# Kernel tuning notes

Measured on AMD Instinct MI355X. Metric: run time of the kernel, lower is better.

Reference implementation:

```python
import jax, jax.numpy as jnp
import numpy as np
from jax import lax

TAU = 0.1
TAU_BASE = 0.1
DIR_W = 1.0
N_LEVELS = 3  # labels has N_LEVELS hierarchy cols + 1 direction col
B, D = 4096, 1024


def setup_inputs() -> dict:
    key = jax.random.key(0)
    k1, k2 = jax.random.split(key)
    embeddings = jax.random.normal(k1, (B, D), dtype=jnp.float32)
    labels = jax.random.randint(k2, (B, N_LEVELS + 1), 0, 8, dtype=jnp.int64)
    return {"embeddings": embeddings, "labels": labels}


def _hier_loss(embeddings, labels):
    # F.normalize(dim=1) with eps=1e-12
    norm = jnp.linalg.norm(embeddings, axis=1, keepdims=True)
    z = embeddings / jnp.maximum(norm, 1e-12)
    hier = labels[:, :-1]          # [B, n_levels]
    dirs = labels[:, -1]           # [B]
    n_levels = hier.shape[1]
    b = z.shape[0]
    eye = jnp.eye(b, dtype=bool)

    sim = (z @ z.T) / TAU                                   # [B, B]
    sim = sim - lax.stop_gradient(jnp.max(sim, axis=1, keepdims=True))
    diff_dir = (dirs[:, None] != dirs[None, :])
    sim = sim - DIR_W * diff_dir.astype(sim.dtype)
    sim = jnp.where(eye, -jnp.inf, sim)
    tiny = jnp.finfo(sim.dtype).tiny
    log_prob = sim - jnp.log(jnp.maximum(jnp.exp(sim).sum(axis=1, keepdims=True), tiny))

    same_dir = ~diff_dir
    total = jnp.zeros((), dtype=sim.dtype)
    max_lower = jnp.full((), -jnp.inf, dtype=sim.dtype)
    seen = jnp.zeros((), dtype=jnp.int32)

    for lvl in range(1, n_levels + 1):  # small fixed loop over hierarchy levels
        same_up_to = jnp.all(hier[:, None, :lvl] == hier[None, :, :lvl], axis=2)  # [B, B]
        pos_mask = same_up_to & same_dir & ~eye
        pos_counts = pos_mask.sum(axis=1)                   # [B] int
        valid = pos_counts > 0
        num_valid = valid.sum()
        any_valid = num_valid > 0

        masked_logp = jnp.where(pos_mask, log_prob, 0.0)
        per_row = masked_logp.sum(axis=1) / jnp.maximum(pos_counts, 1).astype(sim.dtype)
        mean_logp_pos = jnp.sum(jnp.where(valid, per_row, 0.0)) / jnp.maximum(num_valid, 1).astype(sim.dtype)
        raw_loss = -(TAU / TAU_BASE) * mean_logp_pos

        # hmce: running max over levels (max_lower is detached)
        level_loss = jnp.maximum(max_lower, raw_loss)
        max_lower = jnp.where(any_valid,
                              lax.stop_gradient(jnp.maximum(max_lower, level_loss)),
                              max_lower)
        penalty = 2.0 ** (1.0 / lvl)  # h_penalty(1/lvl)
        total = total + jnp.where(any_valid, level_loss * penalty, 0.0)
        seen = seen + any_valid.astype(jnp.int32)

    return total / jnp.maximum(seen, 1).astype(total.dtype)


def reference(embeddings, labels):
    return _hier_loss(embeddings, labels)
```

## Files before the change

### kernel.cpp

```cpp
#include <hip/hip_runtime.h>
#include <hip/hip_bf16.h>
#include <stdint.h>

#define NB 4096
#define ND 1024

typedef __attribute__((ext_vector_type(4))) float f32x4;
typedef __attribute__((ext_vector_type(2))) long i64x2;

__global__ __launch_bounds__(256) void prep_kernel(
    const float* __restrict__ emb, const int* __restrict__ labels,
    unsigned char* __restrict__ zq, int* __restrict__ keys)
{
    const int wid = threadIdx.x >> 6, lane = threadIdx.x & 63;
    const int row = blockIdx.x * 4 + wid;
    const float4* src = (const float4*)(emb + (size_t)row * ND) + lane * 4;
    float4 v[4];
    float ss = 0.0f;
    #pragma unroll
    for (int j = 0; j < 4; ++j) {
        v[j] = src[j];
        ss += v[j].x * v[j].x + v[j].y * v[j].y + v[j].z * v[j].z + v[j].w * v[j].w;
    }
    #pragma unroll
    for (int o = 1; o < 64; o <<= 1) ss += __shfl_xor(ss, o);
    const float inv = 1.0f / fmaxf(sqrtf(ss), 1e-12f);

    int p0 = 0, p1 = 0, p2 = 0, p3 = 0;
    p0 = __builtin_amdgcn_cvt_pk_fp8_f32(v[0].x * inv, v[0].y * inv, p0, false);
    p0 = __builtin_amdgcn_cvt_pk_fp8_f32(v[0].z * inv, v[0].w * inv, p0, true);
    p1 = __builtin_amdgcn_cvt_pk_fp8_f32(v[1].x * inv, v[1].y * inv, p1, false);
    p1 = __builtin_amdgcn_cvt_pk_fp8_f32(v[1].z * inv, v[1].w * inv, p1, true);
    p2 = __builtin_amdgcn_cvt_pk_fp8_f32(v[2].x * inv, v[2].y * inv, p2, false);
    p2 = __builtin_amdgcn_cvt_pk_fp8_f32(v[2].z * inv, v[2].w * inv, p2, true);
    p3 = __builtin_amdgcn_cvt_pk_fp8_f32(v[3].x * inv, v[3].y * inv, p3, false);
    p3 = __builtin_amdgcn_cvt_pk_fp8_f32(v[3].z * inv, v[3].w * inv, p3, true);

    const int sf  = (row >> 4) * 16 + (lane >> 2);
    const int sel = (lane >> 1) & 1;
    const int c0  = (lane & 1) * 2;
    const int L0  = (row & 15) + 16 * c0;
    unsigned char* d = zq + (size_t)sf * 1024;
    int2 w01; w01.x = p0; w01.y = p1;
    int2 w23; w23.x = p2; w23.y = p3;
    *(int2*)(d + L0 * 16 + sel * 8)        = w01;
    *(int2*)(d + (L0 + 16) * 16 + sel * 8) = w23;

    if (lane == 0) {
        const int* lr = labels + row * 4;
        keys[row] = ((lr[3] & 7) << 24) | ((lr[0] & 7) << 16) |
                    ((lr[1] & 7) << 8)  |  (lr[2] & 7);
    }
}

__global__ __launch_bounds__(64, 4) void simtile_kernel(
    const unsigned char* __restrict__ zq, const int* __restrict__ keys,
    float* __restrict__ partials)
{
    const int b = blockIdx.x;
    const int p = (b & 7) * 260 + (b >> 3);
    int r = (int)((sqrtf(8.0f * p + 1.0f) - 1.0f) * 0.5f);
    while ((r + 1) * (r + 2) / 2 <= p) ++r;
    while (r * (r + 1) / 2 > p) --r;
    const int bi = p - r * (r + 1) / 2;
    const int bj = r;
    const int I0 = bi * 64, J0 = bj * 64;
    const bool offdiag = (bi != bj);
    const bool diag = !offdiag;

    const int lane = threadIdx.x;
    const int llo = lane & 15, lhi = lane >> 4;

    __shared__ int keyI[64];
    __shared__ int keyJ[64];
    keyI[lane] = keys[I0 + lane];
    keyJ[lane] = keys[J0 + lane];
    __syncthreads();

    const unsigned char* aF = zq + (size_t)(bi * 4) * 16384 + lane * 16;
    const unsigned char* bF = zq + (size_t)(bj * 4) * 16384 + lane * 16;

    f32x4 acc[4][4];
    #pragma unroll
    for (int m = 0; m < 4; ++m)
        #pragma unroll
        for (int n = 0; n < 4; ++n)
            acc[m][n] = (f32x4){0.f, 0.f, 0.f, 0.f};

    #pragma unroll 1
    for (int t = 0; t < 16; ++t) {
        i64x2 a[4], bb[4];
        #pragma unroll
        for (int m = 0; m < 4; ++m)
            a[m] = *(const i64x2*)(aF + (size_t)m * 16384 + (size_t)t * 1024);
        #pragma unroll
        for (int n = 0; n < 4; ++n)
            bb[n] = *(const i64x2*)(bF + (size_t)n * 16384 + (size_t)t * 1024);
        #pragma unroll
        for (int m = 0; m < 4; ++m)
            #pragma unroll
            for (int n = 0; n < 4; ++n) {
                acc[m][n] = __builtin_amdgcn_mfma_f32_16x16x32_fp8_fp8(
                    a[m][0], bb[n][0], acc[m][n], 0, 0, 0);
                acc[m][n] = __builtin_amdgcn_mfma_f32_16x16x32_fp8_fp8(
                    a[m][1], bb[n][1], acc[m][n], 0, 0, 0);
            }
    }

    int kJ[4], tcol[4];
    #pragma unroll
    for (int n = 0; n < 4; ++n) {
        tcol[n] = n * 16 + llo;
        kJ[n] = keyJ[tcol[n]];
    }

    float stB[4][4];
    #pragma unroll
    for (int n = 0; n < 4; ++n)
        #pragma unroll
        for (int s = 0; s < 4; ++s) stB[n][s] = 0.0f;

    #pragma unroll
    for (int m = 0; m < 4; ++m) {
        float stA[4][4];
        #pragma unroll
        for (int rr = 0; rr < 4; ++rr)
            #pragma unroll
            for (int s = 0; s < 4; ++s) stA[rr][s] = 0.0f;

        int kI[4], trow[4];
        #pragma unroll
        for (int rr = 0; rr < 4; ++rr) {
            trow[rr] = m * 16 + lhi * 4 + rr;
            kI[rr] = keyI[trow[rr]];
        }
        #pragma unroll
        for (int n = 0; n < 4; ++n) {
            #pragma unroll
            for (int rr = 0; rr < 4; ++rr) {
                const float v = acc[m][n][rr] * 10.0f;
                const int x = kI[rr] ^ kJ[n];
                const float pen = (x & 0xFF000000) ? 1.0f : 0.0f;
                const float g = __expf(v - 10.0f - pen);
                if (!(diag && trow[rr] == tcol[n])) {
                    stA[rr][0] += g;           stB[n][0] += g;
                    if ((x & 0xFFFF0000) == 0) { stA[rr][1] += v; stB[n][1] += v; }
                    if ((x & 0xFFFFFF00) == 0) { stA[rr][2] += v; stB[n][2] += v; }
                    if (x == 0)                { stA[rr][3] += v; stB[n][3] += v; }
                }
            }
        }
        #pragma unroll
        for (int rr = 0; rr < 4; ++rr)
            #pragma unroll
            for (int s = 0; s < 4; ++s) {
                float vv = stA[rr][s];
                vv += __shfl_xor(vv, 1);
                vv += __shfl_xor(vv, 2);
                vv += __shfl_xor(vv, 4);
                vv += __shfl_xor(vv, 8);
                stA[rr][s] = vv;
            }
        if (llo == 0) {
            #pragma unroll
            for (int rr = 0; rr < 4; ++rr) {
                float4 o; o.x = stA[rr][0]; o.y = stA[rr][1]; o.z = stA[rr][2]; o.w = stA[rr][3];
                *(float4*)(partials + ((size_t)bj * NB + I0 + trow[rr]) * 4) = o;
            }
        }
    }
    #pragma unroll
    for (int n = 0; n < 4; ++n)
        #pragma unroll
        for (int s = 0; s < 4; ++s) {
            float vv = stB[n][s];
            vv += __shfl_xor(vv, 16);
            vv += __shfl_xor(vv, 32);
            stB[n][s] = vv;
        }
    if (lhi == 0 && offdiag) {
        #pragma unroll
        for (int n = 0; n < 4; ++n) {
            float4 o; o.x = stB[n][0]; o.y = stB[n][1]; o.z = stB[n][2]; o.w = stB[n][3];
            *(float4*)(partials + ((size_t)bi * NB + J0 + tcol[n]) * 4) = o;
        }
    }
}

__global__ __launch_bounds__(256) void rowreduce_kernel(
    const float* __restrict__ partials, const int* __restrict__ keys,
    float* __restrict__ blocksums)
{
    const int tid = threadIdx.x;
    const int row = blockIdx.x * 256 + tid;
    const int lane = tid & 63, wid = tid >> 6;

    __shared__ int h3[4096];
    __shared__ int h2[512];
    __shared__ int h1[64];

    for (int i = tid; i < 4096; i += 256) h3[i] = 0;
    __syncthreads();
    for (int i = tid; i < 4096; i += 256) {
        const int k = keys[i];
        const int i3 = (((((k >> 24) & 7) * 8 + ((k >> 16) & 7)) * 8 + ((k >> 8) & 7)) * 8) + (k & 7);
        atomicAdd(&h3[i3], 1);
    }
    __syncthreads();
    for (int i = tid; i < 512; i += 256) {
        int s = 0;
        #pragma unroll
        for (int j = 0; j < 8; ++j) s += h3[i * 8 + j];
        h2[i] = s;
    }
    __syncthreads();
    if (tid < 64) {
        int s = 0;
        #pragma unroll
        for (int j = 0; j < 8; ++j) s += h2[tid * 8 + j];
        h1[tid] = s;
    }
    __syncthreads();

    float G = 0.f, T1 = 0.f, T2 = 0.f, T3 = 0.f;
    for (int ct = 0; ct < 64; ++ct) {
        const float4 u = *(const float4*)(partials + ((size_t)ct * NB + row) * 4);
        G += u.x; T1 += u.y; T2 += u.z; T3 += u.w;
    }
    const float lg = logf(fmaxf(G, 1e-30f)) + 10.0f;

    const int key = keys[row];
    const int i1 = ((key >> 24) & 7) * 8 + ((key >> 16) & 7);
    const int i2 = i1 * 8 + ((key >> 8) & 7);
    const int i3 = i2 * 8 + (key & 7);
    const int C[3] = {h1[i1] - 1, h2[i2] - 1, h3[i3] - 1};
    const float T[3] = {T1, T2, T3};

    float vals[6];
    #pragma unroll
    for (int l = 0; l < 3; ++l) {
        const bool valid = C[l] > 0;
        const float pr = T[l] / fmaxf((float)C[l], 1.0f) - lg;
        vals[2 * l]     = valid ? pr : 0.0f;
        vals[2 * l + 1] = valid ? 1.0f : 0.0f;
    }

    __shared__ float red[4][6];
    #pragma unroll
    for (int s = 0; s < 6; ++s) {
        float v = vals[s];
        #pragma unroll
        for (int o = 32; o > 0; o >>= 1) v += __shfl_xor(v, o);
        vals[s] = v;
    }
    if (lane == 0)
        #pragma unroll
        for (int s = 0; s < 6; ++s) red[wid][s] = vals[s];
    __syncthreads();
    if (tid == 0) {
        #pragma unroll
        for (int s = 0; s < 6; ++s)
            blocksums[blockIdx.x * 8 + s] = red[0][s] + red[1][s] + red[2][s] + red[3][s];
    }
}

__global__ void final_kernel(const float* __restrict__ blocksums, float* __restrict__ out)
{
    if (threadIdx.x != 0) return;
    float sums[6] = {0, 0, 0, 0, 0, 0};
    for (int b = 0; b < 16; ++b)
        for (int s = 0; s < 6; ++s) sums[s] += blocksums[b * 8 + s];

    const float pen[3] = {2.0f, 1.41421356237309515f, 1.25992104989487319f};
    float total = 0.0f, max_lower = -INFINITY;
    int seen = 0;
    for (int l = 0; l < 3; ++l) {
        const float nv   = sums[2 * l + 1];
        const bool  any  = nv > 0.0f;
        const float mean = sums[2 * l] / fmaxf(nv, 1.0f);
        const float raw  = -mean;
        const float lvl  = fmaxf(max_lower, raw);
        if (any) {
            total += lvl * pen[l];
            max_lower = fmaxf(max_lower, lvl);
            seen++;
        }
    }
    out[0] = total / (float)(seen > 0 ? seen : 1);
}

extern "C" void kernel_launch(void* const* d_in, const int* in_sizes, int n_in,
                              void* d_out, int out_size, void* d_ws, size_t ws_size,
                              hipStream_t stream)
{
    const float* emb    = (const float*)d_in[0];
    const int*   labels = (const int*)d_in[1];
    float*       out    = (float*)d_out;
    char*        ws     = (char*)d_ws;

    unsigned char* zq    = (unsigned char*)(ws);
    int*   keys     = (int*)(ws + 4194304);
    float* partials = (float*)(ws + 4210688);
    float* bsums    = (float*)(ws + 8404992);

    prep_kernel<<<NB / 4, 256, 0, stream>>>(emb, labels, zq, keys);
    simtile_kernel<<<2080, 64, 0, stream>>>(zq, keys, partials);
    rowreduce_kernel<<<NB / 256, 256, 0, stream>>>(partials, keys, bsums);
    final_kernel<<<1, 64, 0, stream>>>(bsums, out);
}
```

Measured before the change: 55.50 us.

## Use 128x128 tiles with four waves sharing double-buffered LDS fp8 panels

The similarity kernel moves from 64x64 tiles handled by one wave to 128x128 tiles handled by four waves. Each wave stages part of the A/B fp8 panels through double-buffered shared memory, so operands are shared across waves instead of each wave reading them from global memory. Per-row partial statistics are combined in shared memory before being written out, which halves the partials buffer and the row-reduce loop. The cost is fewer blocks (528), barrier overhead on every k-step, and more diagonal-tile waste.

Measured after the change: 51.41 us. 7.4% less time.

```diff
diff --git a/kernel.cpp b/kernel.cpp
--- a/kernel.cpp
+++ b/kernel.cpp
@@ -53,32 +53,54 @@
     }
 }
 
-__global__ __launch_bounds__(64, 4) void simtile_kernel(
+__global__ __launch_bounds__(256, 2) void simtile_kernel(
     const unsigned char* __restrict__ zq, const int* __restrict__ keys,
     float* __restrict__ partials)
 {
     const int b = blockIdx.x;
-    const int p = (b & 7) * 260 + (b >> 3);
+    const int p = (b & 7) * 66 + (b >> 3);
     int r = (int)((sqrtf(8.0f * p + 1.0f) - 1.0f) * 0.5f);
     while ((r + 1) * (r + 2) / 2 <= p) ++r;
     while (r * (r + 1) / 2 > p) --r;
     const int bi = p - r * (r + 1) / 2;
     const int bj = r;
-    const int I0 = bi * 64, J0 = bj * 64;
+    const int I0 = bi * 128, J0 = bj * 128;
     const bool offdiag = (bi != bj);
     const bool diag = !offdiag;
 
-    const int lane = threadIdx.x;
+    const int tid = threadIdx.x;
+    const int lane = tid & 63, w = tid >> 6;
     const int llo = lane & 15, lhi = lane >> 4;
-
-    __shared__ int keyI[64];
-    __shared__ int keyJ[64];
-    keyI[lane] = keys[I0 + lane];
-    keyJ[lane] = keys[J0 + lane];
-    __syncthreads();
-
-    const unsigned char* aF = zq + (size_t)(bi * 4) * 16384 + lane * 16;
-    const unsigned char* bF = zq + (size_t)(bj * 4) * 16384 + lane * 16;
+    const int wm = w >> 1, wn = w & 1;
+
+    __shared__ __align__(16) unsigned char sfb[2][16][1024];
+    __shared__ float epiA[2][128][4];
+    __shared__ float epiB[2][128][4];
+    __shared__ int keyI[128];
+    __shared__ int keyJ[128];
+
+    if (tid < 128) {
+        keyI[tid] = keys[I0 + tid];
+        keyJ[tid] = keys[J0 + tid];
+    }
+
+    const unsigned char* gpanel = (w < 2)
+        ? (zq + (size_t)(bi * 8 + w * 4) * 16384 + lane * 16)
+        : (zq + (size_t)(bj * 8 + (w - 2) * 4) * 16384 + lane * 16);
+
+    i64x2 stg[4];
+    #define GLOADU(T)                                                              \
+        do {                                                                       \
+            _Pragma("unroll")                                                      \
+            for (int q = 0; q < 4; ++q)                                            \
+                stg[q] = *(const i64x2*)(gpanel + (size_t)q * 16384 + (T) * 1024); \
+        } while (0)
+    #define DSWRITE(B)                                                             \
+        do {                                                                       \
+            _Pragma("unroll")                                                      \
+            for (int q = 0; q < 4; ++q)                                            \
+                *(i64x2*)(&sfb[B][w * 4 + q][lane * 16]) = stg[q];                 \
+        } while (0)
 
     f32x4 acc[4][4];
     #pragma unroll
@@ -87,15 +109,21 @@
         for (int n = 0; n < 4; ++n)
             acc[m][n] = (f32x4){0.f, 0.f, 0.f, 0.f};
 
+    GLOADU(0);
+    DSWRITE(0);
+    __syncthreads();
+
     #pragma unroll 1
     for (int t = 0; t < 16; ++t) {
+        const int buf = t & 1;
         i64x2 a[4], bb[4];
         #pragma unroll
         for (int m = 0; m < 4; ++m)
-            a[m] = *(const i64x2*)(aF + (size_t)m * 16384 + (size_t)t * 1024);
+            a[m] = *(const i64x2*)(&sfb[buf][wm * 4 + m][lane * 16]);
         #pragma unroll
         for (int n = 0; n < 4; ++n)
-            bb[n] = *(const i64x2*)(bF + (size_t)n * 16384 + (size_t)t * 1024);
+            bb[n] = *(const i64x2*)(&sfb[buf][8 + wn * 4 + n][lane * 16]);
+        if (t < 15) GLOADU(t + 1);
         #pragma unroll
         for (int m = 0; m < 4; ++m)
             #pragma unroll
@@ -105,12 +133,16 @@
                 acc[m][n] = __builtin_amdgcn_mfma_f32_16x16x32_fp8_fp8(
                     a[m][1], bb[n][1], acc[m][n], 0, 0, 0);
             }
-    }
+        if (t < 15) DSWRITE(buf ^ 1);
+        __syncthreads();
+    }
+    #undef GLOADU
+    #undef DSWRITE
 
     int kJ[4], tcol[4];
     #pragma unroll
     for (int n = 0; n < 4; ++n) {
-        tcol[n] = n * 16 + llo;
+        tcol[n] = wn * 64 + n * 16 + llo;
         kJ[n] = keyJ[tcol[n]];
     }
 
@@ -131,7 +163,7 @@
         int kI[4], trow[4];
         #pragma unroll
         for (int rr = 0; rr < 4; ++rr) {
-            trow[rr] = m * 16 + lhi * 4 + rr;
+            trow[rr] = wm * 64 + m * 16 + lhi * 4 + rr;
             kI[rr] = keyI[trow[rr]];
         }
         #pragma unroll
@@ -165,7 +197,7 @@
             #pragma unroll
             for (int rr = 0; rr < 4; ++rr) {
                 float4 o; o.x = stA[rr][0]; o.y = stA[rr][1]; o.z = stA[rr][2]; o.w = stA[rr][3];
-                *(float4*)(partials + ((size_t)bj * NB + I0 + trow[rr]) * 4) = o;
+                *(float4*)&epiA[wn][trow[rr]][0] = o;
             }
         }
     }
@@ -178,11 +210,25 @@
             vv += __shfl_xor(vv, 32);
             stB[n][s] = vv;
         }
-    if (lhi == 0 && offdiag) {
+    if (lhi == 0) {
         #pragma unroll
         for (int n = 0; n < 4; ++n) {
             float4 o; o.x = stB[n][0]; o.y = stB[n][1]; o.z = stB[n][2]; o.w = stB[n][3];
-            *(float4*)(partials + ((size_t)bi * NB + J0 + tcol[n]) * 4) = o;
+            *(float4*)&epiB[wm][tcol[n]][0] = o;
+        }
+    }
+    __syncthreads();
+
+    if (tid < 128) {
+        const float4 a0 = *(const float4*)&epiA[0][tid][0];
+        const float4 a1 = *(const float4*)&epiA[1][tid][0];
+        float4 o; o.x = a0.x + a1.x; o.y = a0.y + a1.y; o.z = a0.z + a1.z; o.w = a0.w + a1.w;
+        *(float4*)(partials + ((size_t)bj * NB + I0 + tid) * 4) = o;
+        if (offdiag) {
+            const float4 b0 = *(const float4*)&epiB[0][tid][0];
+            const float4 b1 = *(const float4*)&epiB[1][tid][0];
+            float4 q; q.x = b0.x + b1.x; q.y = b0.y + b1.y; q.z = b0.z + b1.z; q.w = b0.w + b1.w;
+            *(float4*)(partials + ((size_t)bi * NB + J0 + tid) * 4) = q;
         }
     }
 }
@@ -223,7 +269,7 @@
     __syncthreads();
 
     float G = 0.f, T1 = 0.f, T2 = 0.f, T3 = 0.f;
-    for (int ct = 0; ct < 64; ++ct) {
+    for (int ct = 0; ct < 32; ++ct) {
         const float4 u = *(const float4*)(partials + ((size_t)ct * NB + row) * 4);
         G += u.x; T1 += u.y; T2 += u.z; T3 += u.w;
     }
@@ -301,10 +347,10 @@
     unsigned char* zq    = (unsigned char*)(ws);
     int*   keys     = (int*)(ws + 4194304);
     float* partials = (float*)(ws + 4210688);
-    float* bsums    = (float*)(ws + 8404992);
+    float* bsums    = (float*)(ws + 6307840);
 
     prep_kernel<<<NB / 4, 256, 0, stream>>>(emb, labels, zq, keys);
-    simtile_kernel<<<2080, 64, 0, stream>>>(zq, keys, partials);
+    simtile_kernel<<<528, 256, 0, stream>>>(zq, keys, partials);
     rowreduce_kernel<<<NB / 256, 256, 0, stream>>>(partials, keys, bsums);
     final_kernel<<<1, 64, 0, stream>>>(bsums, out);
 }
```
